# Kernel tuning notes

Hardware: AMD Instinct MI355X
Metric: run time of the kernel (lower is better)

Reference implementation:

```python
import jax, jax.numpy as jnp
import numpy as np

B, N, D, H = 8, 1024, 512, 8
DH = D // H


def setup_inputs() -> dict:
    key = jax.random.key(0)
    ks = jax.random.split(key, 7)
    s = 1.0 / np.sqrt(D)
    return {
        "x": jax.random.normal(ks[0], (B, N, D), dtype=jnp.float32),
        "Wq": jax.random.normal(ks[1], (D, D), dtype=jnp.float32) * s,
        "bq": jax.random.normal(ks[2], (D,), dtype=jnp.float32) * 0.01,
        "Wk": jax.random.normal(ks[3], (D, D), dtype=jnp.float32) * s,
        "bk": jax.random.normal(ks[4], (D,), dtype=jnp.float32) * 0.01,
        "Wv": jax.random.normal(ks[5], (D, D), dtype=jnp.float32) * s,
        "bv": jax.random.normal(ks[6], (D,), dtype=jnp.float32) * 0.01,
    }


def reference(x, Wq, bq, Wk, bk, Wv, bv):
    # Q/K/V projections (nn.Linear: x @ W^T + b; here W stored as [in, out])
    q = x @ Wq + bq  # [B, N, D]
    k = x @ Wk + bk
    v = x @ Wv + bv
    # chunk(dim=2)+cat(dim=0) == split channels into H head groups
    q = q.reshape(B, N, H, DH)
    k = k.reshape(B, N, H, DH)
    v = v.reshape(B, N, H, DH)
    # NOTE: original applies NO 1/sqrt(head_dim) scaling
    scores = jnp.einsum("bqhd,bkhd->bhqk", q, k)  # [B, H, N, N]
    weights = jax.nn.softmax(scores, axis=-1)
    y = jnp.einsum("bhqk,bkhd->bqhd", weights, v)  # [B, N, H, DH]
    return y.reshape(B, N, D)
```

## Files before the change

### kernel.cpp

```cpp
#include <hip/hip_runtime.h>
#include <hip/hip_bf16.h>

typedef _Float16 half8 __attribute__((ext_vector_type(8)));
typedef _Float16 half4v __attribute__((ext_vector_type(4)));
typedef __fp16 fp16x2 __attribute__((ext_vector_type(2)));
typedef float floatx4 __attribute__((ext_vector_type(4)));
typedef float floatx16 __attribute__((ext_vector_type(16)));

#define BB 8
#define NN 1024
#define DD 512
#define HH 8
#define DHH 64
#define LOG2E 1.4426950408889634f

#define EXP2F(x) __builtin_amdgcn_exp2f(x)

__device__ __forceinline__ void gload_lds16(const _Float16* g, _Float16* l) {
    __builtin_amdgcn_global_load_lds(
        (const __attribute__((address_space(1))) void*)g,
        (__attribute__((address_space(3))) void*)l, 16, 0, 0);
}

__global__ __launch_bounds__(256) void cvt_kernel(const float* __restrict__ Wq,
                                                  const float* __restrict__ Wk,
                                                  const float* __restrict__ Wv,
                                                  _Float16* __restrict__ Wt) {
    __shared__ __align__(16) _Float16 tb[64][72];
    int t = blockIdx.x;
    int tid = threadIdx.x;
    int which = t >> 6;
    int rem = t & 63;
    int kt = (rem >> 3) * 64, nt = (rem & 7) * 64;
    const float* W = (which == 0) ? Wq : (which == 1) ? Wk : Wv;
    float wscale = (which == 0) ? LOG2E : 1.0f;
    _Float16* Wto = Wt + (size_t)which * DD * DD;
    for (int i = 0; i < 16; i++) {
        int idx = tid + i * 256;
        int r = idx >> 6, c = idx & 63;
        tb[c][r] = (_Float16)(W[(size_t)(kt + r) * DD + nt + c] * wscale);
    }
    __syncthreads();
    for (int i = 0; i < 16; i++) {
        int idx = tid + i * 256;
        int r = idx >> 6, c = idx & 63;
        Wto[(size_t)(nt + r) * DD + kt + c] = tb[r][c];
    }
}

__global__ __launch_bounds__(256) void qkv_gemm_kernel(const float* __restrict__ x,
                                                       const _Float16* __restrict__ Wt,
                                                       const float* __restrict__ bq,
                                                       const float* __restrict__ bk,
                                                       const float* __restrict__ bv,
                                                       _Float16* __restrict__ QKV) {
    __shared__ __align__(16) _Float16 Ws[128 * 32];
    __shared__ __align__(16) _Float16 Xs[128 * 32];

    int which = blockIdx.z;
    const _Float16* Wtw = Wt + (size_t)which * DD * DD;
    const float* bias = (which == 0) ? bq : (which == 1) ? bk : bv;
    const float bscale = (which == 0) ? LOG2E : 1.0f;

    int tid = threadIdx.x;
    int wave = tid >> 6, lane = tid & 63;
    int quad = lane >> 4, l16 = lane & 15;
    int wm = wave >> 1, wn = wave & 1;
    int mBase = blockIdx.x * 128;
    int nBase = blockIdx.y * 128;

    int srow = wave * 32 + (lane >> 2);
    int scol = (lane & 3) * 8;
    const _Float16* wg = Wtw + (size_t)(nBase + srow) * DD + scol;
    const float*    xg = x   + (size_t)(mBase + srow) * DD + scol;
    _Float16* wl = Ws + (wave * 32) * 32;

    floatx4 acc[4][4];
    for (int i = 0; i < 4; i++)
        for (int j = 0; j < 4; j++) acc[i][j] = (floatx4){0.f, 0.f, 0.f, 0.f};

    for (int kk = 0; kk < DD; kk += 32) {
        __syncthreads();
        gload_lds16(wg + kk,           wl);
        gload_lds16(wg + 16 * DD + kk, wl + 16 * 32);
        float4 a0 = *(const float4*)(xg + kk);
        float4 a1 = *(const float4*)(xg + kk + 4);
        float4 b0 = *(const float4*)(xg + 16 * DD + kk);
        float4 b1 = *(const float4*)(xg + 16 * DD + kk + 4);
        half8 ha, hb;
        ha[0] = (_Float16)a0.x; ha[1] = (_Float16)a0.y; ha[2] = (_Float16)a0.z; ha[3] = (_Float16)a0.w;
        ha[4] = (_Float16)a1.x; ha[5] = (_Float16)a1.y; ha[6] = (_Float16)a1.z; ha[7] = (_Float16)a1.w;
        hb[0] = (_Float16)b0.x; hb[1] = (_Float16)b0.y; hb[2] = (_Float16)b0.z; hb[3] = (_Float16)b0.w;
        hb[4] = (_Float16)b1.x; hb[5] = (_Float16)b1.y; hb[6] = (_Float16)b1.z; hb[7] = (_Float16)b1.w;
        *(half8*)&Xs[srow * 32 + scol] = ha;
        *(half8*)&Xs[(srow + 16) * 32 + scol] = hb;
        __syncthreads();

        half8 af[4], bf[4];
        if (which < 2) {
            for (int i = 0; i < 4; i++)
                af[i] = *(const half8*)&Ws[(wm * 64 + i * 16 + l16) * 32 + quad * 8];
            for (int j = 0; j < 4; j++)
                bf[j] = *(const half8*)&Xs[(wn * 64 + j * 16 + l16) * 32 + quad * 8];
        } else {
            for (int i = 0; i < 4; i++)
                af[i] = *(const half8*)&Xs[(wm * 64 + i * 16 + l16) * 32 + quad * 8];
            for (int j = 0; j < 4; j++)
                bf[j] = *(const half8*)&Ws[(wn * 64 + j * 16 + l16) * 32 + quad * 8];
        }
        for (int i = 0; i < 4; i++)
            for (int j = 0; j < 4; j++)
                acc[i][j] = __builtin_amdgcn_mfma_f32_16x16x32_f16(af[i], bf[j], acc[i][j], 0, 0, 0);
    }

    if (which < 2) {
        _Float16* out = QKV + (size_t)which * (BB * NN) * DD;
        for (int i = 0; i < 4; i++) {
            int feat0 = nBase + wm * 64 + i * 16 + quad * 4;
            float4 b4 = *(const float4*)&bias[feat0];
            b4.x *= bscale; b4.y *= bscale; b4.z *= bscale; b4.w *= bscale;
            for (int j = 0; j < 4; j++) {
                int token = mBase + wn * 64 + j * 16 + l16;
                half4v pack;
                pack[0] = (_Float16)(acc[i][j][0] + b4.x);
                pack[1] = (_Float16)(acc[i][j][1] + b4.y);
                pack[2] = (_Float16)(acc[i][j][2] + b4.z);
                pack[3] = (_Float16)(acc[i][j][3] + b4.w);
                *(half4v*)&out[(size_t)token * DD + feat0] = pack;
            }
        }
    } else {
        _Float16* VT = QKV + (size_t)2 * (BB * NN) * DD;
        for (int j = 0; j < 4; j++) {
            int col = nBase + wn * 64 + j * 16 + l16;
            float bval = bias[col];
            for (int i = 0; i < 4; i++) {
                int row0 = mBase + wm * 64 + i * 16 + quad * 4;
                int b = row0 >> 10;
                int n = row0 & 1023;
                half4v pack;
                for (int reg = 0; reg < 4; reg++) pack[reg] = (_Float16)(acc[i][j][reg] + bval);
                *(half4v*)&VT[((size_t)b * 512 + col) * 1024 + n] = pack;
            }
        }
    }
}

__global__ __launch_bounds__(128) void attn_kernel(const _Float16* __restrict__ QKV,
                                                   float* __restrict__ out) {
    const _Float16* Q  = QKV;
    const _Float16* K  = QKV + (size_t)(BB * NN) * DD;
    const _Float16* VT = QKV + (size_t)2 * (BB * NN) * DD;

    __shared__ __align__(16) _Float16 Kt[2][64 * 64];
    __shared__ __align__(16) _Float16 Vt[2][64 * 64];

    int tid = threadIdx.x;
    int wave = tid >> 6, lane = tid & 63;
    int l31 = lane & 31, hf = lane >> 5;
    int xr = l31 & 7;
    int bid = blockIdx.x;
    int b = bid & 7;
    int local = bid >> 3;
    int h = local & 7;
    int qt = local >> 3;

    const _Float16* Qb  = Q + ((size_t)b * NN) * DD + h * DHH;
    const _Float16* Kb  = K + ((size_t)b * NN) * DD + h * DHH;
    const _Float16* VTb = VT + ((size_t)b * 512 + h * 64) * 1024;

    int qrow = qt * 64 + wave * 32 + l31;
    half8 qf[4];
    for (int sl = 0; sl < 4; sl++)
        qf[sl] = *(const half8*)(Qb + (size_t)qrow * DD + sl * 16 + hf * 8);

    floatx16 o0, o1;
    for (int i = 0; i < 16; i++) { o0[i] = 0.f; o1[i] = 0.f; }
    float m_i = 0.0f, l_i = 0.f;

    int srow = lane >> 3;
    int schunk = (lane & 7) ^ srow;
    const _Float16* kg = Kb + (size_t)(wave * 32 + srow) * DD + schunk * 8;
    const _Float16* vg = VTb + (size_t)(wave * 32 + srow) * 1024 + schunk * 8;
    _Float16* kl0 = &Kt[0][(wave * 32) * 64];
    _Float16* vl0 = &Vt[0][(wave * 32) * 64];
    _Float16* kl1 = &Kt[1][(wave * 32) * 64];
    _Float16* vl1 = &Vt[1][(wave * 32) * 64];

    auto STAGE = [&](int kt, _Float16* kl, _Float16* vl) {
        for (int j = 0; j < 4; j++) {
            gload_lds16(kg + (size_t)(kt * 64 + j * 8) * DD, kl + (j * 8) * 64);
            gload_lds16(vg + (size_t)(j * 8) * 1024 + kt * 64, vl + (j * 8) * 64);
        }
    };

    STAGE(0, kl0, vl0);

    for (int kt = 0; kt < 16; kt++) {
        int cur = kt & 1;
        __syncthreads();
        if (kt + 1 < 16)
            STAGE(kt + 1, cur ? kl0 : kl1, cur ? vl0 : vl1);

        const _Float16* Kc = cur ? &Kt[1][0] : &Kt[0][0];
        const _Float16* Vc = cur ? &Vt[1][0] : &Vt[0][0];

        floatx16 s0, s1;
        for (int i = 0; i < 16; i++) { s0[i] = 0.f; s1[i] = 0.f; }
        __builtin_amdgcn_s_setprio(1);
        for (int sl = 0; sl < 4; sl++) {
            int c = sl * 2 + hf;
            half8 kf0 = *(const half8*)&Kc[l31 * 64 + ((c ^ xr) * 8)];
            half8 kf1 = *(const half8*)&Kc[(32 + l31) * 64 + ((c ^ xr) * 8)];
            s0 = __builtin_amdgcn_mfma_f32_32x32x16_f16(kf0, qf[sl], s0, 0, 0, 0);
            s1 = __builtin_amdgcn_mfma_f32_32x32x16_f16(kf1, qf[sl], s1, 0, 0, 0);
        }
        __builtin_amdgcn_s_setprio(0);

        float mx = s0[0];
        for (int i = 1; i < 16; i++) mx = fmaxf(mx, s0[i]);
        for (int i = 0; i < 16; i++) mx = fmaxf(mx, s1[i]);

        for (int i = 0; i < 16; i++) s0[i] = EXP2F(s0[i] - m_i);
        for (int i = 0; i < 16; i++) s1[i] = EXP2F(s1[i] - m_i);
        float rs = 0.f;
        for (int i = 0; i < 16; i++) rs += s0[i];
        for (int i = 0; i < 16; i++) rs += s1[i];

        mx = fmaxf(mx, __shfl_xor(mx, 32, 64));
        rs += __shfl_xor(rs, 32, 64);

        if (__any(mx > m_i + 11.5443f)) {
            float mnew = fmaxf(m_i, mx);
            float al = EXP2F(m_i - mnew);
            m_i = mnew;
            l_i *= al;
            rs *= al;
            for (int i = 0; i < 16; i++) {
                s0[i] *= al; s1[i] *= al;
                o0[i] *= al; o1[i] *= al;
            }
        }
        l_i += rs;

        __builtin_amdgcn_s_setprio(1);
        {
            for (int sub = 0; sub < 2; sub++) {
                const floatx16& S = sub ? s1 : s0;
                for (int h16 = 0; h16 < 2; h16++) {
                    fp16x2 p0 = __builtin_amdgcn_cvt_pkrtz(S[h16 * 8 + 0], S[h16 * 8 + 1]);
                    fp16x2 p1 = __builtin_amdgcn_cvt_pkrtz(S[h16 * 8 + 2], S[h16 * 8 + 3]);
                    fp16x2 p2 = __builtin_amdgcn_cvt_pkrtz(S[h16 * 8 + 4], S[h16 * 8 + 5]);
                    fp16x2 p3 = __builtin_amdgcn_cvt_pkrtz(S[h16 * 8 + 6], S[h16 * 8 + 7]);
                    half8 pf;
                    pf[0] = (_Float16)p0[0]; pf[1] = (_Float16)p0[1];
                    pf[2] = (_Float16)p1[0]; pf[3] = (_Float16)p1[1];
                    pf[4] = (_Float16)p2[0]; pf[5] = (_Float16)p2[1];
                    pf[6] = (_Float16)p3[0]; pf[7] = (_Float16)p3[1];
                    int c1 = sub * 4 + h16 * 2;
                    {
                        const _Float16* base = &Vc[l31 * 64];
                        half4v v0 = *(const half4v*)(base + ((c1 ^ xr) * 8) + 4 * hf);
                        half4v v1 = *(const half4v*)(base + (((c1 + 1) ^ xr) * 8) + 4 * hf);
                        half8 vf;
                        vf[0] = v0[0]; vf[1] = v0[1]; vf[2] = v0[2]; vf[3] = v0[3];
                        vf[4] = v1[0]; vf[5] = v1[1]; vf[6] = v1[2]; vf[7] = v1[3];
                        o0 = __builtin_amdgcn_mfma_f32_32x32x16_f16(vf, pf, o0, 0, 0, 0);
                    }
                    {
                        const _Float16* base = &Vc[(32 + l31) * 64];
                        half4v v0 = *(const half4v*)(base + ((c1 ^ xr) * 8) + 4 * hf);
                        half4v v1 = *(const half4v*)(base + (((c1 + 1) ^ xr) * 8) + 4 * hf);
                        half8 vf;
                        vf[0] = v0[0]; vf[1] = v0[1]; vf[2] = v0[2]; vf[3] = v0[3];
                        vf[4] = v1[0]; vf[5] = v1[1]; vf[6] = v1[2]; vf[7] = v1[3];
                        o1 = __builtin_amdgcn_mfma_f32_32x32x16_f16(vf, pf, o1, 0, 0, 0);
                    }
                }
            }
        }
        __builtin_amdgcn_s_setprio(0);
    }

    float inv = 1.0f / l_i;
    float* outb = out + ((size_t)b * NN) * DD + h * DHH;
    for (int g = 0; g < 4; g++) {
        float4 st;
        st.x = o0[g * 4 + 0] * inv; st.y = o0[g * 4 + 1] * inv;
        st.z = o0[g * 4 + 2] * inv; st.w = o0[g * 4 + 3] * inv;
        *(float4*)&outb[(size_t)qrow * DD + g * 8 + 4 * hf] = st;
    }
    for (int g = 0; g < 4; g++) {
        float4 st;
        st.x = o1[g * 4 + 0] * inv; st.y = o1[g * 4 + 1] * inv;
        st.z = o1[g * 4 + 2] * inv; st.w = o1[g * 4 + 3] * inv;
        *(float4*)&outb[(size_t)qrow * DD + 32 + g * 8 + 4 * hf] = st;
    }
}

extern "C" void kernel_launch(void* const* d_in, const int* in_sizes, int n_in,
                              void* d_out, int out_size, void* d_ws, size_t ws_size,
                              hipStream_t stream) {
    const float* x  = (const float*)d_in[0];
    const float* Wq = (const float*)d_in[1];
    const float* bq = (const float*)d_in[2];
    const float* Wk = (const float*)d_in[3];
    const float* bk = (const float*)d_in[4];
    const float* Wv = (const float*)d_in[5];
    const float* bv = (const float*)d_in[6];
    float* out = (float*)d_out;

    _Float16* Wt  = (_Float16*)d_ws;
    _Float16* QKV = Wt + (size_t)3 * DD * DD;

    hipLaunchKernelGGL(cvt_kernel, dim3(192), dim3(256), 0, stream,
                       Wq, Wk, Wv, Wt);
    hipLaunchKernelGGL(qkv_gemm_kernel, dim3(64, 4, 3), dim3(256), 0, stream,
                       x, Wt, bq, bk, bv, QKV);
    hipLaunchKernelGGL(attn_kernel, dim3(1024), dim3(128), 0, stream, QKV, out);
}
```

Before: 134.6 us.

## Triple-buffer K/V tiles in attention with explicit vmcnt waits

Moves the attention kernel from double to triple buffering of the K and V LDS tiles. Two tiles are prefetched ahead, and the loop is unrolled by three with fixed buffer indices. The full __syncthreads is replaced by s_waitcnt vmcnt(8) plus s_barrier, so only the oldest outstanding stage must land before compute and global-to-LDS loads can overlap more. In exchange, LDS per block grows by half, which may reduce how many blocks fit on a CU.

```diff
diff --git a/kernel.cpp b/kernel.cpp
--- a/kernel.cpp
+++ b/kernel.cpp
@@ -15,6 +15,8 @@
 #define LOG2E 1.4426950408889634f
 
 #define EXP2F(x) __builtin_amdgcn_exp2f(x)
+
+#define WAITVM(n) asm volatile("s_waitcnt vmcnt(" #n ")" ::: "memory")
 
 __device__ __forceinline__ void gload_lds16(const _Float16* g, _Float16* l) {
     __builtin_amdgcn_global_load_lds(
@@ -152,8 +154,8 @@
     const _Float16* K  = QKV + (size_t)(BB * NN) * DD;
     const _Float16* VT = QKV + (size_t)2 * (BB * NN) * DD;
 
-    __shared__ __align__(16) _Float16 Kt[2][64 * 64];
-    __shared__ __align__(16) _Float16 Vt[2][64 * 64];
+    __shared__ __align__(16) _Float16 Kt[3][64 * 64];
+    __shared__ __align__(16) _Float16 Vt[3][64 * 64];
 
     int tid = threadIdx.x;
     int wave = tid >> 6, lane = tid & 63;
@@ -182,10 +184,9 @@
     int schunk = (lane & 7) ^ srow;
     const _Float16* kg = Kb + (size_t)(wave * 32 + srow) * DD + schunk * 8;
     const _Float16* vg = VTb + (size_t)(wave * 32 + srow) * 1024 + schunk * 8;
-    _Float16* kl0 = &Kt[0][(wave * 32) * 64];
-    _Float16* vl0 = &Vt[0][(wave * 32) * 64];
-    _Float16* kl1 = &Kt[1][(wave * 32) * 64];
-    _Float16* vl1 = &Vt[1][(wave * 32) * 64];
+
+    _Float16* klb[3] = { &Kt[0][(wave * 32) * 64], &Kt[1][(wave * 32) * 64], &Kt[2][(wave * 32) * 64] };
+    _Float16* vlb[3] = { &Vt[0][(wave * 32) * 64], &Vt[1][(wave * 32) * 64], &Vt[2][(wave * 32) * 64] };
 
     auto STAGE = [&](int kt, _Float16* kl, _Float16* vl) {
         for (int j = 0; j < 4; j++) {
@@ -194,17 +195,7 @@
         }
     };
 
-    STAGE(0, kl0, vl0);
-
-    for (int kt = 0; kt < 16; kt++) {
-        int cur = kt & 1;
-        __syncthreads();
-        if (kt + 1 < 16)
-            STAGE(kt + 1, cur ? kl0 : kl1, cur ? vl0 : vl1);
-
-        const _Float16* Kc = cur ? &Kt[1][0] : &Kt[0][0];
-        const _Float16* Vc = cur ? &Vt[1][0] : &Vt[0][0];
-
+    auto COMPUTE = [&](const _Float16* Kc, const _Float16* Vc) {
         floatx16 s0, s1;
         for (int i = 0; i < 16; i++) { s0[i] = 0.f; s1[i] = 0.f; }
         __builtin_amdgcn_s_setprio(1);
@@ -244,43 +235,67 @@
         l_i += rs;
 
         __builtin_amdgcn_s_setprio(1);
-        {
-            for (int sub = 0; sub < 2; sub++) {
-                const floatx16& S = sub ? s1 : s0;
-                for (int h16 = 0; h16 < 2; h16++) {
-                    fp16x2 p0 = __builtin_amdgcn_cvt_pkrtz(S[h16 * 8 + 0], S[h16 * 8 + 1]);
-                    fp16x2 p1 = __builtin_amdgcn_cvt_pkrtz(S[h16 * 8 + 2], S[h16 * 8 + 3]);
-                    fp16x2 p2 = __builtin_amdgcn_cvt_pkrtz(S[h16 * 8 + 4], S[h16 * 8 + 5]);
-                    fp16x2 p3 = __builtin_amdgcn_cvt_pkrtz(S[h16 * 8 + 6], S[h16 * 8 + 7]);
-                    half8 pf;
-                    pf[0] = (_Float16)p0[0]; pf[1] = (_Float16)p0[1];
-                    pf[2] = (_Float16)p1[0]; pf[3] = (_Float16)p1[1];
-                    pf[4] = (_Float16)p2[0]; pf[5] = (_Float16)p2[1];
-                    pf[6] = (_Float16)p3[0]; pf[7] = (_Float16)p3[1];
-                    int c1 = sub * 4 + h16 * 2;
-                    {
-                        const _Float16* base = &Vc[l31 * 64];
-                        half4v v0 = *(const half4v*)(base + ((c1 ^ xr) * 8) + 4 * hf);
-                        half4v v1 = *(const half4v*)(base + (((c1 + 1) ^ xr) * 8) + 4 * hf);
-                        half8 vf;
-                        vf[0] = v0[0]; vf[1] = v0[1]; vf[2] = v0[2]; vf[3] = v0[3];
-                        vf[4] = v1[0]; vf[5] = v1[1]; vf[6] = v1[2]; vf[7] = v1[3];
-                        o0 = __builtin_amdgcn_mfma_f32_32x32x16_f16(vf, pf, o0, 0, 0, 0);
-                    }
-                    {
-                        const _Float16* base = &Vc[(32 + l31) * 64];
-                        half4v v0 = *(const half4v*)(base + ((c1 ^ xr) * 8) + 4 * hf);
-                        half4v v1 = *(const half4v*)(base + (((c1 + 1) ^ xr) * 8) + 4 * hf);
-                        half8 vf;
-                        vf[0] = v0[0]; vf[1] = v0[1]; vf[2] = v0[2]; vf[3] = v0[3];
-                        vf[4] = v1[0]; vf[5] = v1[1]; vf[6] = v1[2]; vf[7] = v1[3];
-                        o1 = __builtin_amdgcn_mfma_f32_32x32x16_f16(vf, pf, o1, 0, 0, 0);
-                    }
+        for (int sub = 0; sub < 2; sub++) {
+            const floatx16& S = sub ? s1 : s0;
+            for (int h16 = 0; h16 < 2; h16++) {
+                fp16x2 p0 = __builtin_amdgcn_cvt_pkrtz(S[h16 * 8 + 0], S[h16 * 8 + 1]);
+                fp16x2 p1 = __builtin_amdgcn_cvt_pkrtz(S[h16 * 8 + 2], S[h16 * 8 + 3]);
+                fp16x2 p2 = __builtin_amdgcn_cvt_pkrtz(S[h16 * 8 + 4], S[h16 * 8 + 5]);
+                fp16x2 p3 = __builtin_amdgcn_cvt_pkrtz(S[h16 * 8 + 6], S[h16 * 8 + 7]);
+                half8 pf;
+                pf[0] = (_Float16)p0[0]; pf[1] = (_Float16)p0[1];
+                pf[2] = (_Float16)p1[0]; pf[3] = (_Float16)p1[1];
+                pf[4] = (_Float16)p2[0]; pf[5] = (_Float16)p2[1];
+                pf[6] = (_Float16)p3[0]; pf[7] = (_Float16)p3[1];
+                int c1 = sub * 4 + h16 * 2;
+                {
+                    const _Float16* base = &Vc[l31 * 64];
+                    half4v v0 = *(const half4v*)(base + ((c1 ^ xr) * 8) + 4 * hf);
+                    half4v v1 = *(const half4v*)(base + (((c1 + 1) ^ xr) * 8) + 4 * hf);
+                    half8 vf;
+                    vf[0] = v0[0]; vf[1] = v0[1]; vf[2] = v0[2]; vf[3] = v0[3];
+                    vf[4] = v1[0]; vf[5] = v1[1]; vf[6] = v1[2]; vf[7] = v1[3];
+                    o0 = __builtin_amdgcn_mfma_f32_32x32x16_f16(vf, pf, o0, 0, 0, 0);
+                }
+                {
+                    const _Float16* base = &Vc[(32 + l31) * 64];
+                    half4v v0 = *(const half4v*)(base + ((c1 ^ xr) * 8) + 4 * hf);
+                    half4v v1 = *(const half4v*)(base + (((c1 + 1) ^ xr) * 8) + 4 * hf);
+                    half8 vf;
+                    vf[0] = v0[0]; vf[1] = v0[1]; vf[2] = v0[2]; vf[3] = v0[3];
+                    vf[4] = v1[0]; vf[5] = v1[1]; vf[6] = v1[2]; vf[7] = v1[3];
+                    o1 = __builtin_amdgcn_mfma_f32_32x32x16_f16(vf, pf, o1, 0, 0, 0);
                 }
             }
         }
         __builtin_amdgcn_s_setprio(0);
-    }
+    };
+
+    STAGE(0, klb[0], vlb[0]);
+    STAGE(1, klb[1], vlb[1]);
+
+    for (int t = 0; t < 5; t++) {
+        int kt = 3 * t;
+        WAITVM(8);
+        __builtin_amdgcn_s_barrier();
+        __builtin_amdgcn_sched_barrier(0);
+        if (kt + 2 < 16) STAGE(kt + 2, klb[2], vlb[2]);
+        COMPUTE(&Kt[0][0], &Vt[0][0]);
+        WAITVM(8);
+        __builtin_amdgcn_s_barrier();
+        __builtin_amdgcn_sched_barrier(0);
+        if (kt + 3 < 16) STAGE(kt + 3, klb[0], vlb[0]);
+        COMPUTE(&Kt[1][0], &Vt[1][0]);
+        WAITVM(8);
+        __builtin_amdgcn_s_barrier();
+        __builtin_amdgcn_sched_barrier(0);
+        if (kt + 4 < 16) STAGE(kt + 4, klb[1], vlb[1]);
+        COMPUTE(&Kt[2][0], &Vt[2][0]);
+    }
+    WAITVM(0);
+    __builtin_amdgcn_s_barrier();
+    __builtin_amdgcn_sched_barrier(0);
+    COMPUTE(&Kt[0][0], &Vt[0][0]);
 
     float inv = 1.0f / l_i;
     float* outb = out + ((size_t)b * NN) * DD + h * DHH;
```

After: 146.9 us. 9.1% more time.

## Split attention KV range across wave pairs and merge partial softmax results

Applied to the files above, without the earlier changes.

The attention block grows from 2 to 4 waves. Each pair of waves handles half of the 16 key/value tiles for the same 64 query rows, and the two partial outputs are merged through LDS using a max/sum rescale at the end. This doubles the waves working on each query tile, aiming to raise occupancy and latency hiding. In exchange it drops the double-buffered prefetch: each iteration now loads its tile and waits on two barriers before computing, and it adds an LDS reduction epilogue.

```diff
diff --git a/kernel.cpp b/kernel.cpp
--- a/kernel.cpp
+++ b/kernel.cpp
@@ -146,7 +146,7 @@
     }
 }
 
-__global__ __launch_bounds__(128) void attn_kernel(const _Float16* __restrict__ QKV,
+__global__ __launch_bounds__(256) void attn_kernel(const _Float16* __restrict__ QKV,
                                                    float* __restrict__ out) {
     const _Float16* Q  = QKV;
     const _Float16* K  = QKV + (size_t)(BB * NN) * DD;
@@ -157,6 +157,7 @@
 
     int tid = threadIdx.x;
     int wave = tid >> 6, lane = tid & 63;
+    int qsub = wave & 1, khalf = wave >> 1;
     int l31 = lane & 31, hf = lane >> 5;
     int xr = l31 & 7;
     int bid = blockIdx.x;
@@ -169,7 +170,7 @@
     const _Float16* Kb  = K + ((size_t)b * NN) * DD + h * DHH;
     const _Float16* VTb = VT + ((size_t)b * 512 + h * 64) * 1024;
 
-    int qrow = qt * 64 + wave * 32 + l31;
+    int qrow = qt * 64 + qsub * 32 + l31;
     half8 qf[4];
     for (int sl = 0; sl < 4; sl++)
         qf[sl] = *(const half8*)(Qb + (size_t)qrow * DD + sl * 16 + hf * 8);
@@ -180,30 +181,22 @@
 
     int srow = lane >> 3;
     int schunk = (lane & 7) ^ srow;
-    const _Float16* kg = Kb + (size_t)(wave * 32 + srow) * DD + schunk * 8;
-    const _Float16* vg = VTb + (size_t)(wave * 32 + srow) * 1024 + schunk * 8;
-    _Float16* kl0 = &Kt[0][(wave * 32) * 64];
-    _Float16* vl0 = &Vt[0][(wave * 32) * 64];
-    _Float16* kl1 = &Kt[1][(wave * 32) * 64];
-    _Float16* vl1 = &Vt[1][(wave * 32) * 64];
-
-    auto STAGE = [&](int kt, _Float16* kl, _Float16* vl) {
+    const _Float16* kg = Kb + (size_t)(qsub * 32 + srow) * DD + schunk * 8;
+    const _Float16* vg = VTb + (size_t)(qsub * 32 + srow) * 1024 + schunk * 8;
+    _Float16* kl = &Kt[khalf][(qsub * 32) * 64];
+    _Float16* vl = &Vt[khalf][(qsub * 32) * 64];
+
+    const _Float16* Kc = &Kt[khalf][0];
+    const _Float16* Vc = &Vt[khalf][0];
+
+    for (int t = 0; t < 8; t++) {
+        int gt = khalf * 8 + t;
+        __syncthreads();
         for (int j = 0; j < 4; j++) {
-            gload_lds16(kg + (size_t)(kt * 64 + j * 8) * DD, kl + (j * 8) * 64);
-            gload_lds16(vg + (size_t)(j * 8) * 1024 + kt * 64, vl + (j * 8) * 64);
-        }
-    };
-
-    STAGE(0, kl0, vl0);
-
-    for (int kt = 0; kt < 16; kt++) {
-        int cur = kt & 1;
+            gload_lds16(kg + (size_t)(gt * 64 + j * 8) * DD, kl + (j * 8) * 64);
+            gload_lds16(vg + (size_t)(j * 8) * 1024 + gt * 64, vl + (j * 8) * 64);
+        }
         __syncthreads();
-        if (kt + 1 < 16)
-            STAGE(kt + 1, cur ? kl0 : kl1, cur ? vl0 : vl1);
-
-        const _Float16* Kc = cur ? &Kt[1][0] : &Kt[0][0];
-        const _Float16* Vc = cur ? &Vt[1][0] : &Vt[0][0];
 
         floatx16 s0, s1;
         for (int i = 0; i < 16; i++) { s0[i] = 0.f; s1[i] = 0.f; }
@@ -244,57 +237,80 @@
         l_i += rs;
 
         __builtin_amdgcn_s_setprio(1);
-        {
-            for (int sub = 0; sub < 2; sub++) {
-                const floatx16& S = sub ? s1 : s0;
-                for (int h16 = 0; h16 < 2; h16++) {
-                    fp16x2 p0 = __builtin_amdgcn_cvt_pkrtz(S[h16 * 8 + 0], S[h16 * 8 + 1]);
-                    fp16x2 p1 = __builtin_amdgcn_cvt_pkrtz(S[h16 * 8 + 2], S[h16 * 8 + 3]);
-                    fp16x2 p2 = __builtin_amdgcn_cvt_pkrtz(S[h16 * 8 + 4], S[h16 * 8 + 5]);
-                    fp16x2 p3 = __builtin_amdgcn_cvt_pkrtz(S[h16 * 8 + 6], S[h16 * 8 + 7]);
-                    half8 pf;
-                    pf[0] = (_Float16)p0[0]; pf[1] = (_Float16)p0[1];
-                    pf[2] = (_Float16)p1[0]; pf[3] = (_Float16)p1[1];
-                    pf[4] = (_Float16)p2[0]; pf[5] = (_Float16)p2[1];
-                    pf[6] = (_Float16)p3[0]; pf[7] = (_Float16)p3[1];
-                    int c1 = sub * 4 + h16 * 2;
-                    {
-                        const _Float16* base = &Vc[l31 * 64];
-                        half4v v0 = *(const half4v*)(base + ((c1 ^ xr) * 8) + 4 * hf);
-                        half4v v1 = *(const half4v*)(base + (((c1 + 1) ^ xr) * 8) + 4 * hf);
-                        half8 vf;
-                        vf[0] = v0[0]; vf[1] = v0[1]; vf[2] = v0[2]; vf[3] = v0[3];
-                        vf[4] = v1[0]; vf[5] = v1[1]; vf[6] = v1[2]; vf[7] = v1[3];
-                        o0 = __builtin_amdgcn_mfma_f32_32x32x16_f16(vf, pf, o0, 0, 0, 0);
-                    }
-                    {
-                        const _Float16* base = &Vc[(32 + l31) * 64];
-                        half4v v0 = *(const half4v*)(base + ((c1 ^ xr) * 8) + 4 * hf);
-                        half4v v1 = *(const half4v*)(base + (((c1 + 1) ^ xr) * 8) + 4 * hf);
-                        half8 vf;
-                        vf[0] = v0[0]; vf[1] = v0[1]; vf[2] = v0[2]; vf[3] = v0[3];
-                        vf[4] = v1[0]; vf[5] = v1[1]; vf[6] = v1[2]; vf[7] = v1[3];
-                        o1 = __builtin_amdgcn_mfma_f32_32x32x16_f16(vf, pf, o1, 0, 0, 0);
-                    }
+        for (int sub = 0; sub < 2; sub++) {
+            const floatx16& S = sub ? s1 : s0;
+            for (int h16 = 0; h16 < 2; h16++) {
+                fp16x2 p0 = __builtin_amdgcn_cvt_pkrtz(S[h16 * 8 + 0], S[h16 * 8 + 1]);
+                fp16x2 p1 = __builtin_amdgcn_cvt_pkrtz(S[h16 * 8 + 2], S[h16 * 8 + 3]);
+                fp16x2 p2 = __builtin_amdgcn_cvt_pkrtz(S[h16 * 8 + 4], S[h16 * 8 + 5]);
+                fp16x2 p3 = __builtin_amdgcn_cvt_pkrtz(S[h16 * 8 + 6], S[h16 * 8 + 7]);
+                half8 pf;
+                pf[0] = (_Float16)p0[0]; pf[1] = (_Float16)p0[1];
+                pf[2] = (_Float16)p1[0]; pf[3] = (_Float16)p1[1];
+                pf[4] = (_Float16)p2[0]; pf[5] = (_Float16)p2[1];
+                pf[6] = (_Float16)p3[0]; pf[7] = (_Float16)p3[1];
+                int c1 = sub * 4 + h16 * 2;
+                {
+                    const _Float16* base = &Vc[l31 * 64];
+                    half4v v0 = *(const half4v*)(base + ((c1 ^ xr) * 8) + 4 * hf);
+                    half4v v1 = *(const half4v*)(base + (((c1 + 1) ^ xr) * 8) + 4 * hf);
+                    half8 vf;
+                    vf[0] = v0[0]; vf[1] = v0[1]; vf[2] = v0[2]; vf[3] = v0[3];
+                    vf[4] = v1[0]; vf[5] = v1[1]; vf[6] = v1[2]; vf[7] = v1[3];
+                    o0 = __builtin_amdgcn_mfma_f32_32x32x16_f16(vf, pf, o0, 0, 0, 0);
+                }
+                {
+                    const _Float16* base = &Vc[(32 + l31) * 64];
+                    half4v v0 = *(const half4v*)(base + ((c1 ^ xr) * 8) + 4 * hf);
+                    half4v v1 = *(const half4v*)(base + (((c1 + 1) ^ xr) * 8) + 4 * hf);
+                    half8 vf;
+                    vf[0] = v0[0]; vf[1] = v0[1]; vf[2] = v0[2]; vf[3] = v0[3];
+                    vf[4] = v1[0]; vf[5] = v1[1]; vf[6] = v1[2]; vf[7] = v1[3];
+                    o1 = __builtin_amdgcn_mfma_f32_32x32x16_f16(vf, pf, o1, 0, 0, 0);
                 }
             }
         }
         __builtin_amdgcn_s_setprio(0);
     }
 
-    float inv = 1.0f / l_i;
-    float* outb = out + ((size_t)b * NN) * DD + h * DHH;
-    for (int g = 0; g < 4; g++) {
-        float4 st;
-        st.x = o0[g * 4 + 0] * inv; st.y = o0[g * 4 + 1] * inv;
-        st.z = o0[g * 4 + 2] * inv; st.w = o0[g * 4 + 3] * inv;
-        *(float4*)&outb[(size_t)qrow * DD + g * 8 + 4 * hf] = st;
-    }
-    for (int g = 0; g < 4; g++) {
-        float4 st;
-        st.x = o1[g * 4 + 0] * inv; st.y = o1[g * 4 + 1] * inv;
-        st.z = o1[g * 4 + 2] * inv; st.w = o1[g * 4 + 3] * inv;
-        *(float4*)&outb[(size_t)qrow * DD + 32 + g * 8 + 4 * hf] = st;
+    float* scA = (float*)&Kt[0][0];
+    float* scB = (float*)&Vt[0][0];
+    __syncthreads();
+    if (wave >= 2) {
+        int bA = ((wave - 2) * 64 + lane) * 16;
+        int bB = ((wave - 2) * 64 + lane) * 18;
+        for (int i = 0; i < 16; i++) scA[bA + i] = o0[i];
+        for (int i = 0; i < 16; i++) scB[bB + i] = o1[i];
+        scB[bB + 16] = m_i;
+        scB[bB + 17] = l_i;
+    }
+    __syncthreads();
+    if (wave < 2) {
+        int bA = (wave * 64 + lane) * 16;
+        int bB = (wave * 64 + lane) * 18;
+        float pm = scB[bB + 16], pl = scB[bB + 17];
+        float M = fmaxf(m_i, pm);
+        float a = EXP2F(m_i - M);
+        float bw = EXP2F(pm - M);
+        float lm = l_i * a + pl * bw;
+        float inv = 1.0f / lm;
+        float* outb = out + ((size_t)b * NN) * DD + h * DHH;
+        for (int g = 0; g < 4; g++) {
+            float4 st;
+            st.x = (o0[g * 4 + 0] * a + scA[bA + g * 4 + 0] * bw) * inv;
+            st.y = (o0[g * 4 + 1] * a + scA[bA + g * 4 + 1] * bw) * inv;
+            st.z = (o0[g * 4 + 2] * a + scA[bA + g * 4 + 2] * bw) * inv;
+            st.w = (o0[g * 4 + 3] * a + scA[bA + g * 4 + 3] * bw) * inv;
+            *(float4*)&outb[(size_t)qrow * DD + g * 8 + 4 * hf] = st;
+        }
+        for (int g = 0; g < 4; g++) {
+            float4 st;
+            st.x = (o1[g * 4 + 0] * a + scB[bB + g * 4 + 0] * bw) * inv;
+            st.y = (o1[g * 4 + 1] * a + scB[bB + g * 4 + 1] * bw) * inv;
+            st.z = (o1[g * 4 + 2] * a + scB[bB + g * 4 + 2] * bw) * inv;
+            st.w = (o1[g * 4 + 3] * a + scB[bB + g * 4 + 3] * bw) * inv;
+            *(float4*)&outb[(size_t)qrow * DD + 32 + g * 8 + 4 * hf] = st;
+        }
     }
 }
 
@@ -317,5 +333,5 @@
                        Wq, Wk, Wv, Wt);
     hipLaunchKernelGGL(qkv_gemm_kernel, dim3(64, 4, 3), dim3(256), 0, stream,
                        x, Wt, bq, bk, bv, QKV);
-    hipLaunchKernelGGL(attn_kernel, dim3(1024), dim3(128), 0, stream, QKV, out);
-}
+    hipLaunchKernelGGL(attn_kernel, dim3(1024), dim3(256), 0, stream, QKV, out);
+}
```

Result: no change. 135.0 us (+0.3%).
